# Optimization experiments

Measured on AMD Instinct MI355X. Metric: run time of the kernel, lower is better.

The kernel has to match this reference:

```python
import jax, jax.numpy as jnp
import numpy as np
import math

B, S, IN, H, M = 4, 2048, 256, 128, 128  # mem_dim must equal hidden_size


def _xavier(key, shape):
    fan_in, fan_out = shape[0], shape[-1]
    lim = math.sqrt(6.0 / (fan_in + fan_out))
    return jax.random.uniform(key, shape, jnp.float32, -lim, lim)


def setup_inputs() -> dict:
    key = jax.random.key(0)
    ks = jax.random.split(key, 8)
    return dict(
        x=jax.random.normal(ks[0], (B, S, IN), jnp.float32),
        c0=jnp.zeros((M, M), jnp.float32),   # init_hidden matrix memory
        n0=jnp.zeros((M, 1), jnp.float32),   # init_hidden normalizer
        w_q=_xavier(ks[1], (IN, H)), b_q=jnp.zeros((H,), jnp.float32),
        w_k=_xavier(ks[2], (IN, M)), b_k=jnp.zeros((M,), jnp.float32),
        w_v=_xavier(ks[3], (IN, M)), b_v=jnp.zeros((M,), jnp.float32),
        w_i=_xavier(ks[4], (IN, 1)), b_i=jnp.zeros((1,), jnp.float32),
        w_f=_xavier(ks[5], (IN, 1)), b_f=jnp.zeros((1,), jnp.float32),
        w_o=_xavier(ks[6], (IN, H)), b_o=jnp.zeros((H,), jnp.float32),
    )


def reference(x, c0, n0, w_q, b_q, w_k, b_k, w_v, b_v, w_i, b_i, w_f, b_f, w_o, b_o):
    Bb, Ss, Ii = x.shape
    Mm = w_k.shape[1]
    Hh = w_q.shape[1]
    xf = x.reshape(Bb * Ss, Ii)                                  # [N, IN]
    q = xf @ w_q + b_q                                           # [N, H]
    k = (xf @ w_k + b_k) * (1.0 / math.sqrt(Mm))                 # [N, M]
    v = xf @ w_v + b_v                                           # [N, M]
    i_t = jnp.exp(xf @ w_i + b_i)                                # [N, 1]
    f_t = jax.nn.sigmoid(xf @ w_f + b_f)                         # [N, 1]
    # Original loop never updates c_prev: c_t[n] = f[n]*c0 + i[n]*outer(v[n], k[n])
    c = f_t[:, :, None] * c0[None] + i_t[:, :, None] * (v[:, :, None] * k[:, None, :])  # [N, M, M]
    n = f_t[:, :, None] * n0[None] + i_t[:, :, None] * k[:, :, None]                    # [N, M, 1]
    c = c.reshape(Bb, Ss, Mm, Mm)
    n = n.reshape(Bb, Ss, Mm, 1)
    q4 = q.reshape(Bb, Ss, Hh)
    nq = jnp.einsum('bsm,bsm->bs', n[..., 0], q4)                # n^T q
    denom = jnp.maximum(jnp.abs(nq), 1.0)[..., None]             # max(|n^T q|, 1)
    h_tilde = jnp.einsum('bsmk,bsk->bsm', c, q4) / denom         # (c_t q) / denom
    o = jax.nn.sigmoid(xf @ w_o + b_o).reshape(Bb, Ss, Hh)
    h = o * h_tilde                                              # [B, S, H]
    return (h, c, n)
```

## Files before the change

kernel.cpp:

```cpp
#include <hip/hip_runtime.h>
#include <math.h>

#define B_    4
#define S_    2048
#define IN_   256
#define H_    128
#define M_    128
#define NROWS (B_ * S_)
#define RPB   16
#define GRP   4
#define NGRP  4
#define TPB   512
#define XPAD  260

typedef float f4_t __attribute__((ext_vector_type(4)));

__global__ __launch_bounds__(TPB) void xlstm_pipe(
    const float* __restrict__ x,
    const float* __restrict__ c0,
    const float* __restrict__ n0,
    const float* __restrict__ w_q, const float* __restrict__ b_q,
    const float* __restrict__ w_k, const float* __restrict__ b_k,
    const float* __restrict__ w_v, const float* __restrict__ b_v,
    const float* __restrict__ w_i, const float* __restrict__ b_i,
    const float* __restrict__ w_f, const float* __restrict__ b_f,
    const float* __restrict__ w_o, const float* __restrict__ b_o,
    float* __restrict__ out_h,
    float* __restrict__ out_c,
    float* __restrict__ out_n)
{
    __shared__ float xs[RPB][XPAD];
    __shared__ float bq[2][GRP][M_];
    __shared__ float bk[2][GRP][M_];
    __shared__ float bv[2][GRP][M_];
    __shared__ float bo[2][GRP][M_];
    __shared__ float itf[RPB][2];
    __shared__ float scalb[2][GRP][2];

    const int t    = threadIdx.x;
    const int row0 = blockIdx.x * RPB;
    const bool prod = (t < 256);

    for (int p4 = t; p4 < RPB * IN_ / 4; p4 += TPB) {
        int p = p4 * 4;
        float4 v = *(const float4*)(x + (size_t)row0 * IN_ + p);
        *(float4*)&xs[p >> 8][p & 255] = v;
    }
    __syncthreads();

    const int cg  = t & 31;
    const int mat = (t >> 5) & 3;
    const int rh  = (t >> 7) & 1;
    const int c4  = cg * 4;
    const int col = t & 127;
    const float* W    = (mat==0)? w_q : (mat==1)? w_k : (mat==2)? w_v : w_o;
    const float* BIAS = (mat==0)? b_q : (mat==1)? b_k : (mat==2)? b_v : b_o;
    const f4_t bias4 = *(const f4_t*)(BIAS + c4);
    const float kscale = 0.08838834764831843f;

    const int ct   = t & 255;
    const int base = ct * 4;
    const int jj   = base & 127;

    float c0qA = 0.f, c0qB = 0.f;

    #pragma unroll 1
    for (int s = 0; s <= NGRP; ++s) {
        if (prod) {
            if (s == 0) {
                const int gr = t >> 4, gseg = t & 15;
                const float* xrow = &xs[gr][gseg * 16];
                float pi = 0.f, pf = 0.f;
                #pragma unroll
                for (int u = 0; u < 4; ++u) {
                    float4 xv  = *(const float4*)(xrow + u * 4);
                    float4 wiv = *(const float4*)(w_i + gseg * 16 + u * 4);
                    float4 wfv = *(const float4*)(w_f + gseg * 16 + u * 4);
                    pi = fmaf(xv.x,wiv.x, fmaf(xv.y,wiv.y, fmaf(xv.z,wiv.z, fmaf(xv.w,wiv.w, pi))));
                    pf = fmaf(xv.x,wfv.x, fmaf(xv.y,wfv.y, fmaf(xv.z,wfv.z, fmaf(xv.w,wfv.w, pf))));
                }
                #pragma unroll
                for (int mm = 1; mm < 16; mm <<= 1) { pi += __shfl_xor(pi, mm); pf += __shfl_xor(pf, mm); }
                if (gseg == 0) {
                    itf[gr][0] = __expf(pi + b_i[0]);
                    itf[gr][1] = 1.f / (1.f + __expf(-(pf + b_f[0])));
                }
            }
            if (s > 0) {
                const int b = (s - 1) & 1;
                #pragma unroll
                for (int rr = 0; rr < 2; ++rr) {
                    const int lrow = rh * 2 + rr;
                    const int row  = (s - 1) * GRP + lrow;
                    const size_t grow = (size_t)(row0 + row);
                    const float iv = itf[row][0], fv = itf[row][1];
                    out_n[grow * M_ + col] = fmaf(fv, n0[col], iv * bk[b][lrow][col]);
                    const float kq  = scalb[b][lrow][0];
                    const float n0q = scalb[b][lrow][1];
                    const float nq = fmaf(fv, n0q, iv * kq);
                    const float denom = fmaxf(fabsf(nq), 1.f);
                    const float c0q = rr ? c0qB : c0qA;
                    const float ht = fmaf(fv, c0q, iv * bv[b][lrow][col] * kq) / denom;
                    out_h[grow * H_ + col] = bo[b][lrow][col] * ht;
                }
            }
            if (s < NGRP) {
                const int b  = s & 1;
                const int r0 = s * GRP + rh * 2;
                f4_t acc0 = (f4_t){0.f,0.f,0.f,0.f};
                f4_t acc1 = (f4_t){0.f,0.f,0.f,0.f};
                #pragma unroll 4
                for (int it = 0; it < 64; ++it) {
                    const int k0 = it * 4;
                    const float* wp = W + (size_t)k0 * H_ + c4;
                    f4_t w0 = *(const f4_t*)(wp);
                    f4_t w1 = *(const f4_t*)(wp + H_);
                    f4_t w2 = *(const f4_t*)(wp + 2 * H_);
                    f4_t w3 = *(const f4_t*)(wp + 3 * H_);
                    f4_t xv0 = *(const f4_t*)&xs[r0][k0];
                    f4_t xv1 = *(const f4_t*)&xs[r0 + 1][k0];
                    acc0 += xv0.x*w0 + xv0.y*w1 + xv0.z*w2 + xv0.w*w3;
                    acc1 += xv1.x*w0 + xv1.y*w1 + xv1.z*w2 + xv1.w*w3;
                }
                acc0 += bias4; acc1 += bias4;
                if (mat == 1) { acc0 *= kscale; acc1 *= kscale; }
                if (mat == 3) {
                    acc0.x = 1.f/(1.f+__expf(-acc0.x)); acc0.y = 1.f/(1.f+__expf(-acc0.y));
                    acc0.z = 1.f/(1.f+__expf(-acc0.z)); acc0.w = 1.f/(1.f+__expf(-acc0.w));
                    acc1.x = 1.f/(1.f+__expf(-acc1.x)); acc1.y = 1.f/(1.f+__expf(-acc1.y));
                    acc1.z = 1.f/(1.f+__expf(-acc1.z)); acc1.w = 1.f/(1.f+__expf(-acc1.w));
                }
                float (*DST)[M_] = (mat==0)? bq[b] : (mat==1)? bk[b] : (mat==2)? bv[b] : bo[b];
                const int lr = rh * 2;
                *(f4_t*)&DST[lr][c4]     = acc0;
                *(f4_t*)&DST[lr + 1][c4] = acc1;
            }
        } else if (s > 0) {
            const int b     = (s - 1) & 1;
            const int gbase = (s - 1) * GRP;
            #pragma unroll 2
            for (int ch = 0; ch < 8; ++ch) {
                const int p = (ch << 10) + base;
                const int m = p >> 7;
                f4_t c0v = *(const f4_t*)(c0 + p);
                #pragma unroll
                for (int r = 0; r < GRP; ++r) {
                    const int row = gbase + r;
                    f4_t k4 = *(const f4_t*)&bk[b][r][jj];
                    float sf = itf[row][0] * bv[b][r][m];
                    f4_t o4 = itf[row][1] * c0v + sf * k4;
                    __builtin_nontemporal_store(o4,
                        (f4_t*)(out_c + (size_t)(row0 + row) * (M_ * M_) + p));
                }
            }
        }
        __syncthreads();
        if (prod) {
            if (s < NGRP) {
                const int b  = s & 1;
                const int lr = rh * 2;
                float a0 = 0.f, a1 = 0.f;
                const float* c0row = c0 + (size_t)col * M_;
                #pragma unroll 2
                for (int j4 = 0; j4 < M_; j4 += 4) {
                    f4_t w4 = *(const f4_t*)(c0row + j4);
                    f4_t qa = *(const f4_t*)&bq[b][lr][j4];
                    f4_t qb = *(const f4_t*)&bq[b][lr + 1][j4];
                    a0 = fmaf(w4.x,qa.x, fmaf(w4.y,qa.y, fmaf(w4.z,qa.z, fmaf(w4.w,qa.w, a0))));
                    a1 = fmaf(w4.x,qb.x, fmaf(w4.y,qb.y, fmaf(w4.z,qb.z, fmaf(w4.w,qb.w, a1))));
                }
                c0qA = a0; c0qB = a1;
                const int wv = t >> 6;
                const int l  = t & 63;
                const float ka  = bk[b][wv][l], kb2 = bk[b][wv][l + 64];
                const float qa2 = bq[b][wv][l], qb2 = bq[b][wv][l + 64];
                float pkq = fmaf(ka, qa2, kb2 * qb2);
                float pnq = fmaf(n0[l], qa2, n0[l + 64] * qb2);
                #pragma unroll
                for (int mm = 1; mm < 64; mm <<= 1) { pkq += __shfl_xor(pkq, mm); pnq += __shfl_xor(pnq, mm); }
                if (l == 0) { scalb[b][wv][0] = pkq; scalb[b][wv][1] = pnq; }
            }
        } else if (s > 0) {
            const int b     = (s - 1) & 1;
            const int gbase = (s - 1) * GRP;
            #pragma unroll 2
            for (int ch = 8; ch < 16; ++ch) {
                const int p = (ch << 10) + base;
                const int m = p >> 7;
                f4_t c0v = *(const f4_t*)(c0 + p);
                #pragma unroll
                for (int r = 0; r < GRP; ++r) {
                    const int row = gbase + r;
                    f4_t k4 = *(const f4_t*)&bk[b][r][jj];
                    float sf = itf[row][0] * bv[b][r][m];
                    f4_t o4 = itf[row][1] * c0v + sf * k4;
                    __builtin_nontemporal_store(o4,
                        (f4_t*)(out_c + (size_t)(row0 + row) * (M_ * M_) + p));
                }
            }
        }
        __syncthreads();
    }
}

extern "C" void kernel_launch(void* const* d_in, const int* in_sizes, int n_in,
                              void* d_out, int out_size, void* d_ws, size_t ws_size,
                              hipStream_t stream) {
    const float* x   = (const float*)d_in[0];
    const float* c0  = (const float*)d_in[1];
    const float* n0  = (const float*)d_in[2];
    const float* w_q = (const float*)d_in[3];  const float* b_q = (const float*)d_in[4];
    const float* w_k = (const float*)d_in[5];  const float* b_k = (const float*)d_in[6];
    const float* w_v = (const float*)d_in[7];  const float* b_v = (const float*)d_in[8];
    const float* w_i = (const float*)d_in[9];  const float* b_i = (const float*)d_in[10];
    const float* w_f = (const float*)d_in[11]; const float* b_f = (const float*)d_in[12];
    const float* w_o = (const float*)d_in[13]; const float* b_o = (const float*)d_in[14];

    float* out   = (float*)d_out;
    float* out_h = out;
    float* out_c = out + (size_t)NROWS * H_;
    float* out_n = out_c + (size_t)NROWS * M_ * M_;

    hipLaunchKernelGGL(xlstm_pipe, dim3(NROWS / RPB), dim3(TPB), 0, stream,
                       x, c0, n0, w_q, b_q, w_k, b_k, w_v, b_v,
                       w_i, b_i, w_f, b_f, w_o, b_o,
                       out_h, out_c, out_n);
}
```

Baseline: 141.6 us.

## Rebalance c-tensor store work between producer and writer warps across phases

Writer threads now split the c output by row pairs: rows 0-1 in the first phase and rows 2-3 in the second, each covering chunks 0-11. The producer warps write chunks 12-15 for all four rows of the current group after their scalar reductions. Per-row constants (k vector, gates, output pointers) are hoisted out of the chunk loop. The aim is to give producer threads part of the dominant store traffic so they are not idle, at the cost of more code in the producer path and a changed store pattern.

```diff
diff --git a/kernel.cpp b/kernel.cpp
--- a/kernel.cpp
+++ b/kernel.cpp
@@ -138,20 +138,21 @@
         } else if (s > 0) {
             const int b     = (s - 1) & 1;
             const int gbase = (s - 1) * GRP;
+            f4_t k40 = *(const f4_t*)&bk[b][0][jj];
+            f4_t k41 = *(const f4_t*)&bk[b][1][jj];
+            const float if0 = itf[gbase][0],     ff0 = itf[gbase][1];
+            const float if1 = itf[gbase + 1][0], ff1 = itf[gbase + 1][1];
+            float* o0 = out_c + (size_t)(row0 + gbase)     * (M_ * M_);
+            float* o1 = out_c + (size_t)(row0 + gbase + 1) * (M_ * M_);
             #pragma unroll 2
-            for (int ch = 0; ch < 8; ++ch) {
+            for (int ch = 0; ch < 12; ++ch) {
                 const int p = (ch << 10) + base;
                 const int m = p >> 7;
                 f4_t c0v = *(const f4_t*)(c0 + p);
-                #pragma unroll
-                for (int r = 0; r < GRP; ++r) {
-                    const int row = gbase + r;
-                    f4_t k4 = *(const f4_t*)&bk[b][r][jj];
-                    float sf = itf[row][0] * bv[b][r][m];
-                    f4_t o4 = itf[row][1] * c0v + sf * k4;
-                    __builtin_nontemporal_store(o4,
-                        (f4_t*)(out_c + (size_t)(row0 + row) * (M_ * M_) + p));
-                }
+                f4_t oa = ff0 * c0v + (if0 * bv[b][0][m]) * k40;
+                f4_t ob = ff1 * c0v + (if1 * bv[b][1][m]) * k41;
+                __builtin_nontemporal_store(oa, (f4_t*)(o0 + p));
+                __builtin_nontemporal_store(ob, (f4_t*)(o1 + p));
             }
         }
         __syncthreads();
@@ -179,24 +180,41 @@
                 #pragma unroll
                 for (int mm = 1; mm < 64; mm <<= 1) { pkq += __shfl_xor(pkq, mm); pnq += __shfl_xor(pnq, mm); }
                 if (l == 0) { scalb[b][wv][0] = pkq; scalb[b][wv][1] = pnq; }
+
+                const int gbase = s * GRP;
+                #pragma unroll
+                for (int ch = 12; ch < 16; ++ch) {
+                    const int p = (ch << 10) + base;
+                    const int m = p >> 7;
+                    f4_t c0v = *(const f4_t*)(c0 + p);
+                    #pragma unroll
+                    for (int r = 0; r < GRP; ++r) {
+                        f4_t k4 = *(const f4_t*)&bk[b][r][jj];
+                        float sf = itf[gbase + r][0] * bv[b][r][m];
+                        f4_t o4 = itf[gbase + r][1] * c0v + sf * k4;
+                        __builtin_nontemporal_store(o4,
+                            (f4_t*)(out_c + (size_t)(row0 + gbase + r) * (M_ * M_) + p));
+                    }
+                }
             }
         } else if (s > 0) {
             const int b     = (s - 1) & 1;
             const int gbase = (s - 1) * GRP;
+            f4_t k42 = *(const f4_t*)&bk[b][2][jj];
+            f4_t k43 = *(const f4_t*)&bk[b][3][jj];
+            const float if2 = itf[gbase + 2][0], ff2 = itf[gbase + 2][1];
+            const float if3 = itf[gbase + 3][0], ff3 = itf[gbase + 3][1];
+            float* o2 = out_c + (size_t)(row0 + gbase + 2) * (M_ * M_);
+            float* o3 = out_c + (size_t)(row0 + gbase + 3) * (M_ * M_);
             #pragma unroll 2
-            for (int ch = 8; ch < 16; ++ch) {
+            for (int ch = 0; ch < 12; ++ch) {
                 const int p = (ch << 10) + base;
                 const int m = p >> 7;
                 f4_t c0v = *(const f4_t*)(c0 + p);
-                #pragma unroll
-                for (int r = 0; r < GRP; ++r) {
-                    const int row = gbase + r;
-                    f4_t k4 = *(const f4_t*)&bk[b][r][jj];
-                    float sf = itf[row][0] * bv[b][r][m];
-                    f4_t o4 = itf[row][1] * c0v + sf * k4;
-                    __builtin_nontemporal_store(o4,
-                        (f4_t*)(out_c + (size_t)(row0 + row) * (M_ * M_) + p));
-                }
+                f4_t oa = ff2 * c0v + (if2 * bv[b][2][m]) * k42;
+                f4_t ob = ff3 * c0v + (if3 * bv[b][3][m]) * k43;
+                __builtin_nontemporal_store(oa, (f4_t*)(o2 + p));
+                __builtin_nontemporal_store(ob, (f4_t*)(o3 + p));
             }
         }
         __syncthreads();
```

After: 144.2 us. Within noise of the previous version (+1.8%).
